# Optimization experiments

Measured on AMD Instinct MI355X. Metric: run time of the kernel, lower is better.

The kernel has to match this reference:

```python
import jax, jax.numpy as jnp
import numpy as np

TEMPERATURE = 1.0  # module default current_temperature
TOP_K = 2
NUM_EXPERTS = 64
EPS = 1e-10


def setup_inputs() -> dict:
    key = jax.random.key(0)
    k1, k2 = jax.random.split(key)
    x = jax.random.normal(k1, (4, 4096, 2048), dtype=jnp.float32)
    # nn.Linear(d_model, num_experts) weight has shape [num_experts, d_model]
    W_gate = jax.random.normal(k2, (NUM_EXPERTS, 2048), dtype=jnp.float32) * (1.0 / np.sqrt(2048))
    return {"x": x, "W_gate": W_gate}


def reference(x, W_gate):
    # Gate GEMM: [B,S,D] x [E,D] -> [B,S,E]
    logits = jnp.einsum("bsd,ed->bse", x, W_gate)
    scaled = logits / TEMPERATURE
    # Full distribution over experts (for load-balancing loss)
    router_probs = jax.nn.softmax(scaled, axis=-1)
    # Top-k selection over the expert dim, then renormalize via softmax
    top_k_logits, top_k_indices = jax.lax.top_k(scaled, TOP_K)  # [B,S,K]
    top_k_weights = jax.nn.softmax(top_k_logits, axis=-1)
    # Routing stats (no-grad in torch; plain values here)
    entropy = -jnp.sum(router_probs * jnp.log(router_probs + EPS), axis=-1)
    routing_entropy = entropy.mean()
    selection_confidence = top_k_weights[:, :, 0].mean()
    counts = jnp.zeros((NUM_EXPERTS,), dtype=x.dtype).at[top_k_indices.reshape(-1)].add(1.0)
    expert_utilization = counts / (counts.sum() + EPS)
    return (top_k_weights, top_k_indices, router_probs,
            routing_entropy, selection_confidence, expert_utilization)
```

## Files before the change

### kernel.cpp

```cpp
#include <hip/hip_runtime.h>
#include <math.h>

#define NTOK 16384
#define DIM 2048
#define NEXP 64
#define KG 4
#define NC 16
#define WTOK 32
#define BTOK 128

#define OFF_W    0
#define OFF_I    32768
#define OFF_P    65536
#define OFF_ENT  1114112
#define OFF_CONF 1114113
#define OFF_UTIL 1114114

#define PLG_OFF  196608
#define PLG_STRIDE 1048576
#define WS_NEED_STRIDED (786432ull + 16777216ull)

typedef short s16x8 __attribute__((ext_vector_type(8)));
typedef float f32x4 __attribute__((ext_vector_type(4)));

__device__ __forceinline__ unsigned short f2bf(float v) {
    unsigned u = __builtin_bit_cast(unsigned, v);
    u = u + 0x7FFFu + ((u >> 16) & 1u);
    return (unsigned short)(u >> 16);
}
__device__ __forceinline__ float bf2f(unsigned short b) {
    return __builtin_bit_cast(float, (unsigned)b << 16);
}

__device__ __forceinline__ void gload16(const void* g, void* l) {
    __builtin_amdgcn_global_load_lds(
        (const __attribute__((address_space(1))) unsigned int*)g,
        (__attribute__((address_space(3))) unsigned int*)l, 16, 0, 0);
}

__global__ void router_wsplit(const float* __restrict__ Wg, uint4* __restrict__ wsp,
                              float* __restrict__ out) {
    const int bid = blockIdx.x;
    const int tid = threadIdx.x;
    const int c   = bid >> 2;
    const int gt  = (bid & 3) * 64 + tid;
    if (c == 0 && gt < 66) out[OFF_ENT + gt] = 0.0f;
    const int nt = gt >> 6, l = gt & 63;
    const int e  = 16 * nt + (l & 15);
    const int k0 = 32 * c + 8 * (l >> 4);
    const float* src = Wg + (size_t)e * DIM + k0;
    float4 a = *(const float4*)src;
    float4 b = *(const float4*)(src + 4);
    float v[8] = {a.x, a.y, a.z, a.w, b.x, b.y, b.z, b.w};
    unsigned short H[8], M[8], L[8];
    #pragma unroll
    for (int j = 0; j < 8; ++j) {
        H[j] = f2bf(v[j]);  float r = v[j] - bf2f(H[j]);
        M[j] = f2bf(r);     r = r - bf2f(M[j]);
        L[j] = f2bf(r);
    }
    uint4 ph, pm, pl;
    ph.x = H[0] | ((unsigned)H[1] << 16); ph.y = H[2] | ((unsigned)H[3] << 16);
    ph.z = H[4] | ((unsigned)H[5] << 16); ph.w = H[6] | ((unsigned)H[7] << 16);
    pm.x = M[0] | ((unsigned)M[1] << 16); pm.y = M[2] | ((unsigned)M[3] << 16);
    pm.z = M[4] | ((unsigned)M[5] << 16); pm.w = M[6] | ((unsigned)M[7] << 16);
    pl.x = L[0] | ((unsigned)L[1] << 16); pl.y = L[2] | ((unsigned)L[3] << 16);
    pl.z = L[4] | ((unsigned)L[5] << 16); pl.w = L[6] | ((unsigned)L[7] << 16);
    const int idx = c * 256 + gt;
    wsp[idx]         = ph;
    wsp[16384 + idx] = pm;
    wsp[32768 + idx] = pl;
}

__global__ void router_zero(float* __restrict__ p) {
    ((float4*)p)[blockIdx.x * 256 + threadIdx.x] = make_float4(0.f, 0.f, 0.f, 0.f);
}

#define CONVA3(a0_, a1_) {                                               \
    float xv[8];                                                         \
    xv[0]=a0_.x; xv[1]=a0_.y; xv[2]=a0_.z; xv[3]=a0_.w;                  \
    xv[4]=a1_.x; xv[5]=a1_.y; xv[6]=a1_.z; xv[7]=a1_.w;                  \
    _Pragma("unroll")                                                    \
    for (int j = 0; j < 8; ++j) {                                        \
        unsigned u_  = __builtin_bit_cast(unsigned, xv[j]);              \
        unsigned hb_ = u_ & 0xFFFF0000u;                                 \
        float    r_  = xv[j] - __builtin_bit_cast(float, hb_);           \
        unsigned mb_ = __builtin_bit_cast(unsigned, r_) & 0xFFFF0000u;   \
        float    r2_ = r_ - __builtin_bit_cast(float, mb_);              \
        unsigned lb_ = __builtin_bit_cast(unsigned, r2_);                \
        ah[j] = (short)(hb_ >> 16);                                      \
        am[j] = (short)(mb_ >> 16);                                      \
        al[j] = (short)(lb_ >> 16);                                      \
    } }

#define MF(A_, B_, C_) __builtin_amdgcn_mfma_f32_16x16x32_bf16(A_, B_, C_, 0, 0, 0)
#define BC(q_) __builtin_bit_cast(s16x8, q_)

#define STAGE(c_) { _Pragma("unroll")                                    \
    for (int i_ = 0; i_ < 4; ++i_) {                                     \
        const int tau_ = 8 * i_ + (l >> 3);                              \
        const int gs_  = ((l & 7) >> 1) ^ (tau_ & 3);                    \
        gload16(xw + (size_t)tau_ * DIM + (c_) * 32 + gs_ * 8 + (l & 1) * 4, \
                &ring[wv][(c_) & 3][8 * i_][0]);                         \
    } }

#define READA(tt_, c_) {                                                 \
    const int tau_ = (tt_) * 16 + tr;                                    \
    const int sl_  = qd ^ (tau_ & 3);                                    \
    const uint4* row_ = &ring[wv][(c_) & 3][tau_][0];                    \
    float4 a0_ = __builtin_bit_cast(float4, row_[2 * sl_]);              \
    float4 a1_ = __builtin_bit_cast(float4, row_[2 * sl_ + 1]);          \
    CONVA3(a0_, a1_);                                                    \
    }

#define LOADW12(W_, c_) { const int b_ = (kg * NC + (c_)) * 256 + l;     \
    W_[0] = wq[b_];          W_[1] = wq[b_ + 64];                        \
    W_[2] = wq[b_ + 128];    W_[3] = wq[b_ + 192];                       \
    W_[4] = wq[16384 + b_];       W_[5] = wq[16384 + b_ + 64];           \
    W_[6] = wq[16384 + b_ + 128]; W_[7] = wq[16384 + b_ + 192];          \
    W_[8] = wq[32768 + b_];       W_[9] = wq[32768 + b_ + 64];           \
    W_[10] = wq[32768 + b_ + 128]; W_[11] = wq[32768 + b_ + 192]; }

#define PR4(F_, W_, o_, Q0_, Q1_, Q2_, Q3_) {                            \
    Q0_ = MF(F_, BC(W_[(o_) + 0]), Q0_);                                 \
    Q1_ = MF(F_, BC(W_[(o_) + 1]), Q1_);                                 \
    Q2_ = MF(F_, BC(W_[(o_) + 2]), Q2_);                                 \
    Q3_ = MF(F_, BC(W_[(o_) + 3]), Q3_); }

#define COMPUTE24(W_, Q0_, Q1_, Q2_, Q3_) {                              \
    PR4(ah, W_, 0, Q0_, Q1_, Q2_, Q3_);                                  \
    PR4(am, W_, 0, Q0_, Q1_, Q2_, Q3_);                                  \
    PR4(ah, W_, 4, Q0_, Q1_, Q2_, Q3_);                                  \
    PR4(am, W_, 4, Q0_, Q1_, Q2_, Q3_);                                  \
    PR4(ah, W_, 8, Q0_, Q1_, Q2_, Q3_);                                  \
    PR4(al, W_, 0, Q0_, Q1_, Q2_, Q3_); }

#define PHASE(c_, W_) {                                                  \
    if ((c_) + 3 < NC) STAGE((c_) + 3);                                  \
    asm volatile("s_waitcnt vmcnt(8)" ::: "memory");                     \
    __builtin_amdgcn_sched_barrier(0);                                   \
    READA(0, c_);                                                        \
    COMPUTE24(W_, q00, q01, q02, q03);                                   \
    READA(1, c_);                                                        \
    COMPUTE24(W_, q10, q11, q12, q13);                                   \
    if ((c_) + 2 < NC) LOADW12(W_, (c_) + 2);                            \
    }

template<bool STRIDED>
__global__ __launch_bounds__(256, 2) void router_main(
    const float* __restrict__ x, const uint4* __restrict__ wq,
    float* __restrict__ plg)
{
    __shared__ __align__(16) uint4 ring[4][4][WTOK][8];

    const int tid = threadIdx.x;
    const int l   = tid & 63;
    const int wv  = tid >> 6;
    const int tr  = l & 15;
    const int qd  = l >> 4;
    const int kg  = blockIdx.x & 3;
    const int bt0 = (blockIdx.x >> 2) * BTOK;
    const int t0w = bt0 + wv * WTOK;

    const float* xw = x + (size_t)t0w * DIM + kg * (NC * 32);

    f32x4 q00 = (f32x4)(0.f), q01 = (f32x4)(0.f), q02 = (f32x4)(0.f), q03 = (f32x4)(0.f);
    f32x4 q10 = (f32x4)(0.f), q11 = (f32x4)(0.f), q12 = (f32x4)(0.f), q13 = (f32x4)(0.f);
    s16x8 ah, am, al;
    uint4 wA[12], wB[12];

    STAGE(0); STAGE(1); STAGE(2);
    LOADW12(wA, 0); LOADW12(wB, 1);

    #pragma unroll
    for (int c = 0; c < NC; c += 2) {
        PHASE(c, wA);
        PHASE(c + 1, wB);
    }

    float* dst = STRIDED ? (plg + (size_t)kg * PLG_STRIDE) : plg;
#define STACC(acc_, tt_, nt_) { _Pragma("unroll")                        \
    for (int r = 0; r < 4; ++r) {                                        \
        int tok = t0w + (tt_) * 16 + 4 * qd + r;                         \
        int ex_ = (nt_) * 16 + tr;                                       \
        if constexpr (STRIDED) dst[(size_t)tok * 64 + ex_] = acc_[r];    \
        else atomicAdd(&dst[(size_t)tok * 64 + ex_], acc_[r]);           \
    } }
    STACC(q00, 0, 0); STACC(q01, 0, 1); STACC(q02, 0, 2); STACC(q03, 0, 3);
    STACC(q10, 1, 0); STACC(q11, 1, 1); STACC(q12, 1, 2); STACC(q13, 1, 3);
#undef STACC
}

__device__ __forceinline__ void merge2(float& m1, int& i1, float& m2, int& i2,
                                       float om1, int oi1, float om2, int oi2) {
    bool of = (om1 > m1) || (om1 == m1 && oi1 < i1);
    float n1, n2; int j1, j2;
    if (of) {
        n1 = om1; j1 = oi1;
        bool s = (m1 > om2) || (m1 == om2 && i1 < oi2);
        n2 = s ? m1 : om2; j2 = s ? i1 : oi2;
    } else {
        n1 = m1; j1 = i1;
        bool s = (om1 > m2) || (om1 == m2 && oi1 < i2);
        n2 = s ? om1 : m2; j2 = s ? oi1 : i2;
    }
    m1 = n1; i1 = j1; m2 = n2; i2 = j2;
}

template<int NPART>
__global__ void router_post(const float* __restrict__ plg, float* __restrict__ out) {
    __shared__ float s_ent, s_conf, s_cnt[NEXP];
    const int tid  = threadIdx.x;
    const int lane = tid & 63;
    const int wv   = tid >> 6;
    if (tid == 0) { s_ent = 0.f; s_conf = 0.f; }
    if (tid < NEXP) s_cnt[tid] = 0.f;
    __syncthreads();

    const int tb = blockIdx.x * 32 + wv * 8;
    float entA = 0.f, confA = 0.f;

    for (int k = 0; k < 8; ++k) {
        const int t = tb + k;
        float lgv = 0.f;
        #pragma unroll
        for (int p = 0; p < NPART; ++p)
            lgv += plg[(size_t)p * PLG_STRIDE + (size_t)t * 64 + lane];

        float m1 = lgv, m2 = -INFINITY;
        int   i1 = lane, i2 = 127;
        #pragma unroll
        for (int off = 32; off >= 1; off >>= 1) {
            float om1 = __shfl_xor(m1, off);
            int   oi1 = __shfl_xor(i1, off);
            float om2 = __shfl_xor(m2, off);
            int   oi2 = __shfl_xor(i2, off);
            merge2(m1, i1, m2, i2, om1, oi1, om2, oi2);
        }
        float d  = lgv - m1;
        float ex = __expf(d);
        float ss = ex, ts = d * ex;
        #pragma unroll
        for (int off = 32; off >= 1; off >>= 1) {
            ss += __shfl_xor(ss, off);
            ts += __shfl_xor(ts, off);
        }
        float rs = 1.0f / ss;
        out[OFF_P + (size_t)t * 64 + lane] = ex * rs;
        if (lane == 0) {
            float H  = logf(ss) - ts * rs;
            float e2 = __expf(m2 - m1);
            float rn = 1.0f / (1.0f + e2);
            *(float2*)&out[OFF_W + 2 * t] = make_float2(rn, e2 * rn);
            *(float2*)&out[OFF_I + 2 * t] = make_float2((float)i1, (float)i2);
            entA  += H;
            confA += rn;
            atomicAdd(&s_cnt[i1], 1.0f);
            atomicAdd(&s_cnt[i2], 1.0f);
        }
    }
    if (lane == 0) { atomicAdd(&s_ent, entA); atomicAdd(&s_conf, confA); }
    __syncthreads();
    if (tid == 0) {
        atomicAdd(&out[OFF_ENT],  s_ent  * (1.0f / 16384.0f));
        atomicAdd(&out[OFF_CONF], s_conf * (1.0f / 16384.0f));
    }
    if (tid < NEXP)
        atomicAdd(&out[OFF_UTIL + tid], s_cnt[tid] * (1.0f / 32768.0f));
}

extern "C" void kernel_launch(void* const* d_in, const int* in_sizes, int n_in,
                              void* d_out, int out_size, void* d_ws, size_t ws_size,
                              hipStream_t stream) {
    const float* x  = (const float*)d_in[0];
    const float* Wg = (const float*)d_in[1];
    float* out = (float*)d_out;
    float* plg = (float*)d_ws + PLG_OFF;
    (void)in_sizes; (void)n_in; (void)out_size;

    router_wsplit<<<dim3(256), dim3(64), 0, stream>>>(Wg, (uint4*)d_ws, out);
    if (ws_size >= WS_NEED_STRIDED) {
        router_main<true><<<dim3((NTOK / BTOK) * KG), dim3(256), 0, stream>>>(
            x, (const uint4*)d_ws, plg);
        router_post<KG><<<dim3(512), dim3(256), 0, stream>>>(plg, out);
    } else {
        router_zero<<<dim3(1024), dim3(256), 0, stream>>>(plg);
        router_main<false><<<dim3((NTOK / BTOK) * KG), dim3(256), 0, stream>>>(
            x, (const uint4*)d_ws, plg);
        router_post<1><<<dim3(512), dim3(256), 0, stream>>>(plg, out);
    }
}
```

Baseline: 240.5 us.

## Fuse gate GEMM and softmax/top-k epilogue into one kernel with in-block split-K

Replaces the three-kernel pipeline (weight pre-split, split-K GEMM writing partial logits to workspace, post-processing kernel) with a single kernel. Each block handles 32 tokens, its four waves split the K dimension, reduce their partial logits through shared memory, then run softmax, top-2, entropy and utilisation directly. W is now loaded as fp32 and split into three bf16 parts inside the loop instead of once up front. This drops the partial-logit round trip through global memory and two launches, at the cost of redundant W conversion per block, a shallower double-buffered x ring, and serialized shared-memory reductions.

```diff
diff --git a/kernel.cpp b/kernel.cpp
--- a/kernel.cpp
+++ b/kernel.cpp
@@ -4,10 +4,8 @@
 #define NTOK 16384
 #define DIM 2048
 #define NEXP 64
-#define KG 4
-#define NC 16
 #define WTOK 32
-#define BTOK 128
+#define NCW 16
 
 #define OFF_W    0
 #define OFF_I    32768
@@ -16,10 +14,6 @@
 #define OFF_CONF 1114113
 #define OFF_UTIL 1114114
 
-#define PLG_OFF  196608
-#define PLG_STRIDE 1048576
-#define WS_NEED_STRIDED (786432ull + 16777216ull)
-
 typedef short s16x8 __attribute__((ext_vector_type(8)));
 typedef float f32x4 __attribute__((ext_vector_type(4)));
 
@@ -38,45 +32,19 @@
         (__attribute__((address_space(3))) unsigned int*)l, 16, 0, 0);
 }
 
-__global__ void router_wsplit(const float* __restrict__ Wg, uint4* __restrict__ wsp,
-                              float* __restrict__ out) {
-    const int bid = blockIdx.x;
-    const int tid = threadIdx.x;
-    const int c   = bid >> 2;
-    const int gt  = (bid & 3) * 64 + tid;
-    if (c == 0 && gt < 66) out[OFF_ENT + gt] = 0.0f;
-    const int nt = gt >> 6, l = gt & 63;
-    const int e  = 16 * nt + (l & 15);
-    const int k0 = 32 * c + 8 * (l >> 4);
-    const float* src = Wg + (size_t)e * DIM + k0;
-    float4 a = *(const float4*)src;
-    float4 b = *(const float4*)(src + 4);
-    float v[8] = {a.x, a.y, a.z, a.w, b.x, b.y, b.z, b.w};
-    unsigned short H[8], M[8], L[8];
-    #pragma unroll
-    for (int j = 0; j < 8; ++j) {
-        H[j] = f2bf(v[j]);  float r = v[j] - bf2f(H[j]);
-        M[j] = f2bf(r);     r = r - bf2f(M[j]);
-        L[j] = f2bf(r);
-    }
-    uint4 ph, pm, pl;
-    ph.x = H[0] | ((unsigned)H[1] << 16); ph.y = H[2] | ((unsigned)H[3] << 16);
-    ph.z = H[4] | ((unsigned)H[5] << 16); ph.w = H[6] | ((unsigned)H[7] << 16);
-    pm.x = M[0] | ((unsigned)M[1] << 16); pm.y = M[2] | ((unsigned)M[3] << 16);
-    pm.z = M[4] | ((unsigned)M[5] << 16); pm.w = M[6] | ((unsigned)M[7] << 16);
-    pl.x = L[0] | ((unsigned)L[1] << 16); pl.y = L[2] | ((unsigned)L[3] << 16);
-    pl.z = L[4] | ((unsigned)L[5] << 16); pl.w = L[6] | ((unsigned)L[7] << 16);
-    const int idx = c * 256 + gt;
-    wsp[idx]         = ph;
-    wsp[16384 + idx] = pm;
-    wsp[32768 + idx] = pl;
-}
-
-__global__ void router_zero(float* __restrict__ p) {
-    ((float4*)p)[blockIdx.x * 256 + threadIdx.x] = make_float4(0.f, 0.f, 0.f, 0.f);
-}
-
-#define CONVA3(a0_, a1_) {                                               \
+__global__ void router_init(float* __restrict__ out) {
+    if (threadIdx.x < 66) out[OFF_ENT + threadIdx.x] = 0.0f;
+}
+
+#define STAGE(c_) do { _Pragma("unroll")                                 \
+    for (int i_ = 0; i_ < 4; ++i_) {                                     \
+        const int tau_ = 8 * i_ + (l >> 3);                              \
+        const int gs_  = ((l & 7) >> 1) ^ (tau_ & 3);                    \
+        gload16(xw + (size_t)tau_ * DIM + (c_) * 32 + gs_ * 8 + (l & 1) * 4, \
+                &ring[wv][(c_) & 1][8 * i_][0]);                         \
+    } } while (0)
+
+#define CONVA3(a0_, a1_) do {                                            \
     float xv[8];                                                         \
     xv[0]=a0_.x; xv[1]=a0_.y; xv[2]=a0_.z; xv[3]=a0_.w;                  \
     xv[4]=a1_.x; xv[5]=a1_.y; xv[6]=a1_.z; xv[7]=a1_.w;                  \
@@ -91,105 +59,53 @@
         ah[j] = (short)(hb_ >> 16);                                      \
         am[j] = (short)(mb_ >> 16);                                      \
         al[j] = (short)(lb_ >> 16);                                      \
-    } }
-
-#define MF(A_, B_, C_) __builtin_amdgcn_mfma_f32_16x16x32_bf16(A_, B_, C_, 0, 0, 0)
-#define BC(q_) __builtin_bit_cast(s16x8, q_)
-
-#define STAGE(c_) { _Pragma("unroll")                                    \
-    for (int i_ = 0; i_ < 4; ++i_) {                                     \
-        const int tau_ = 8 * i_ + (l >> 3);                              \
-        const int gs_  = ((l & 7) >> 1) ^ (tau_ & 3);                    \
-        gload16(xw + (size_t)tau_ * DIM + (c_) * 32 + gs_ * 8 + (l & 1) * 4, \
-                &ring[wv][(c_) & 3][8 * i_][0]);                         \
-    } }
-
-#define READA(tt_, c_) {                                                 \
+    } } while (0)
+
+#define READA(tt_, c_) do {                                              \
     const int tau_ = (tt_) * 16 + tr;                                    \
     const int sl_  = qd ^ (tau_ & 3);                                    \
-    const uint4* row_ = &ring[wv][(c_) & 3][tau_][0];                    \
+    const uint4* row_ = &ring[wv][(c_) & 1][tau_][0];                    \
     float4 a0_ = __builtin_bit_cast(float4, row_[2 * sl_]);              \
     float4 a1_ = __builtin_bit_cast(float4, row_[2 * sl_ + 1]);          \
     CONVA3(a0_, a1_);                                                    \
-    }
-
-#define LOADW12(W_, c_) { const int b_ = (kg * NC + (c_)) * 256 + l;     \
-    W_[0] = wq[b_];          W_[1] = wq[b_ + 64];                        \
-    W_[2] = wq[b_ + 128];    W_[3] = wq[b_ + 192];                       \
-    W_[4] = wq[16384 + b_];       W_[5] = wq[16384 + b_ + 64];           \
-    W_[6] = wq[16384 + b_ + 128]; W_[7] = wq[16384 + b_ + 192];          \
-    W_[8] = wq[32768 + b_];       W_[9] = wq[32768 + b_ + 64];           \
-    W_[10] = wq[32768 + b_ + 128]; W_[11] = wq[32768 + b_ + 192]; }
-
-#define PR4(F_, W_, o_, Q0_, Q1_, Q2_, Q3_) {                            \
-    Q0_ = MF(F_, BC(W_[(o_) + 0]), Q0_);                                 \
-    Q1_ = MF(F_, BC(W_[(o_) + 1]), Q1_);                                 \
-    Q2_ = MF(F_, BC(W_[(o_) + 2]), Q2_);                                 \
-    Q3_ = MF(F_, BC(W_[(o_) + 3]), Q3_); }
-
-#define COMPUTE24(W_, Q0_, Q1_, Q2_, Q3_) {                              \
-    PR4(ah, W_, 0, Q0_, Q1_, Q2_, Q3_);                                  \
-    PR4(am, W_, 0, Q0_, Q1_, Q2_, Q3_);                                  \
-    PR4(ah, W_, 4, Q0_, Q1_, Q2_, Q3_);                                  \
-    PR4(am, W_, 4, Q0_, Q1_, Q2_, Q3_);                                  \
-    PR4(ah, W_, 8, Q0_, Q1_, Q2_, Q3_);                                  \
-    PR4(al, W_, 0, Q0_, Q1_, Q2_, Q3_); }
-
-#define PHASE(c_, W_) {                                                  \
-    if ((c_) + 3 < NC) STAGE((c_) + 3);                                  \
-    asm volatile("s_waitcnt vmcnt(8)" ::: "memory");                     \
-    __builtin_amdgcn_sched_barrier(0);                                   \
-    READA(0, c_);                                                        \
-    COMPUTE24(W_, q00, q01, q02, q03);                                   \
-    READA(1, c_);                                                        \
-    COMPUTE24(W_, q10, q11, q12, q13);                                   \
-    if ((c_) + 2 < NC) LOADW12(W_, (c_) + 2);                            \
-    }
-
-template<bool STRIDED>
-__global__ __launch_bounds__(256, 2) void router_main(
-    const float* __restrict__ x, const uint4* __restrict__ wq,
-    float* __restrict__ plg)
-{
-    __shared__ __align__(16) uint4 ring[4][4][WTOK][8];
-
-    const int tid = threadIdx.x;
-    const int l   = tid & 63;
-    const int wv  = tid >> 6;
-    const int tr  = l & 15;
-    const int qd  = l >> 4;
-    const int kg  = blockIdx.x & 3;
-    const int bt0 = (blockIdx.x >> 2) * BTOK;
-    const int t0w = bt0 + wv * WTOK;
-
-    const float* xw = x + (size_t)t0w * DIM + kg * (NC * 32);
-
-    f32x4 q00 = (f32x4)(0.f), q01 = (f32x4)(0.f), q02 = (f32x4)(0.f), q03 = (f32x4)(0.f);
-    f32x4 q10 = (f32x4)(0.f), q11 = (f32x4)(0.f), q12 = (f32x4)(0.f), q13 = (f32x4)(0.f);
-    s16x8 ah, am, al;
-    uint4 wA[12], wB[12];
-
-    STAGE(0); STAGE(1); STAGE(2);
-    LOADW12(wA, 0); LOADW12(wB, 1);
-
-    #pragma unroll
-    for (int c = 0; c < NC; c += 2) {
-        PHASE(c, wA);
-        PHASE(c + 1, wB);
-    }
-
-    float* dst = STRIDED ? (plg + (size_t)kg * PLG_STRIDE) : plg;
-#define STACC(acc_, tt_, nt_) { _Pragma("unroll")                        \
-    for (int r = 0; r < 4; ++r) {                                        \
-        int tok = t0w + (tt_) * 16 + 4 * qd + r;                         \
-        int ex_ = (nt_) * 16 + tr;                                       \
-        if constexpr (STRIDED) dst[(size_t)tok * 64 + ex_] = acc_[r];    \
-        else atomicAdd(&dst[(size_t)tok * 64 + ex_], acc_[r]);           \
-    } }
-    STACC(q00, 0, 0); STACC(q01, 0, 1); STACC(q02, 0, 2); STACC(q03, 0, 3);
-    STACC(q10, 1, 0); STACC(q11, 1, 1); STACC(q12, 1, 2); STACC(q13, 1, 3);
-#undef STACC
-}
+    } while (0)
+
+#define LOADWF(W_, c_) do { _Pragma("unroll")                            \
+    for (int nt_ = 0; nt_ < 4; ++nt_) {                                  \
+        const float* p_ = wsrc + (size_t)nt_ * 16 * DIM + (c_) * 32;     \
+        W_[2 * nt_]     = *(const float4*)(p_);                          \
+        W_[2 * nt_ + 1] = *(const float4*)(p_ + 4);                      \
+    } } while (0)
+
+#define CONVW(a_, b_, BH_, BM_, BL_) do {                                \
+    float wv8[8];                                                        \
+    wv8[0]=a_.x; wv8[1]=a_.y; wv8[2]=a_.z; wv8[3]=a_.w;                  \
+    wv8[4]=b_.x; wv8[5]=b_.y; wv8[6]=b_.z; wv8[7]=b_.w;                  \
+    _Pragma("unroll")                                                    \
+    for (int j = 0; j < 8; ++j) {                                        \
+        unsigned short h_ = f2bf(wv8[j]);                                \
+        float r_  = wv8[j] - bf2f(h_);                                   \
+        unsigned short m_ = f2bf(r_);                                    \
+        float r2_ = r_ - bf2f(m_);                                       \
+        unsigned short lo_ = f2bf(r2_);                                  \
+        BH_[j] = (short)h_; BM_[j] = (short)m_; BL_[j] = (short)lo_;     \
+    } } while (0)
+
+#define MF(A_, B_, C_) __builtin_amdgcn_mfma_f32_16x16x32_bf16(A_, B_, C_, 0, 0, 0)
+
+#define PR4(F_, B_, Q0_, Q1_, Q2_, Q3_) do {                             \
+    Q0_ = MF(F_, B_[0], Q0_);                                            \
+    Q1_ = MF(F_, B_[1], Q1_);                                            \
+    Q2_ = MF(F_, B_[2], Q2_);                                            \
+    Q3_ = MF(F_, B_[3], Q3_); } while (0)
+
+#define COMPUTE24(Q0_, Q1_, Q2_, Q3_) do {                               \
+    PR4(ah, bh, Q0_, Q1_, Q2_, Q3_);                                     \
+    PR4(am, bh, Q0_, Q1_, Q2_, Q3_);                                     \
+    PR4(ah, bm, Q0_, Q1_, Q2_, Q3_);                                     \
+    PR4(am, bm, Q0_, Q1_, Q2_, Q3_);                                     \
+    PR4(ah, bl, Q0_, Q1_, Q2_, Q3_);                                     \
+    PR4(al, bh, Q0_, Q1_, Q2_, Q3_); } while (0)
 
 __device__ __forceinline__ void merge2(float& m1, int& i1, float& m2, int& i2,
                                        float om1, int oi1, float om2, int oi2) {
@@ -207,28 +123,87 @@
     m1 = n1; i1 = j1; m2 = n2; i2 = j2;
 }
 
-template<int NPART>
-__global__ void router_post(const float* __restrict__ plg, float* __restrict__ out) {
+__global__ __launch_bounds__(256, 2) void router_main(
+    const float* __restrict__ x, const float* __restrict__ Wg,
+    float* __restrict__ out)
+{
+    __shared__ __align__(16) uint4 ring[4][2][WTOK][8];
+    __shared__ float lg[WTOK][NEXP + 1];
     __shared__ float s_ent, s_conf, s_cnt[NEXP];
-    const int tid  = threadIdx.x;
-    const int lane = tid & 63;
-    const int wv   = tid >> 6;
+
+    const int tid = threadIdx.x;
+    const int l   = tid & 63;
+    const int wv  = tid >> 6;
+    const int tr  = l & 15;
+    const int qd  = l >> 4;
+    const int t0  = blockIdx.x * WTOK;
+
     if (tid == 0) { s_ent = 0.f; s_conf = 0.f; }
     if (tid < NEXP) s_cnt[tid] = 0.f;
-    __syncthreads();
-
-    const int tb = blockIdx.x * 32 + wv * 8;
+
+    const float* xw   = x  + (size_t)t0 * DIM + wv * (NCW * 32);
+    const float* wsrc = Wg + (size_t)tr * DIM + wv * (NCW * 32) + 8 * qd;
+
+    f32x4 q00 = (f32x4)(0.f), q01 = (f32x4)(0.f), q02 = (f32x4)(0.f), q03 = (f32x4)(0.f);
+    f32x4 q10 = (f32x4)(0.f), q11 = (f32x4)(0.f), q12 = (f32x4)(0.f), q13 = (f32x4)(0.f);
+    s16x8 ah, am, al;
+    s16x8 bh[4], bm[4], bl[4];
+    float4 wA[8], wB[8];
+
+    STAGE(0);
+    LOADWF(wA, 0); LOADWF(wB, 1);
+
+    #pragma unroll
+    for (int c = 0; c < NCW; ++c) {
+        if (c + 1 < NCW) STAGE(c + 1);
+        if (c == NCW - 1) { asm volatile("s_waitcnt vmcnt(0)" ::: "memory"); }
+        else              { asm volatile("s_waitcnt vmcnt(12)" ::: "memory"); }
+        __builtin_amdgcn_sched_barrier(0);
+        {
+            float4* wc = (c & 1) ? wB : wA;
+            #pragma unroll
+            for (int nt = 0; nt < 4; ++nt)
+                CONVW(wc[2 * nt], wc[2 * nt + 1], bh[nt], bm[nt], bl[nt]);
+        }
+        READA(0, c);
+        COMPUTE24(q00, q01, q02, q03);
+        READA(1, c);
+        COMPUTE24(q10, q11, q12, q13);
+        {
+            float4* wn = (c & 1) ? wB : wA;
+            if (c + 2 < NCW) LOADWF(wn, c + 2);
+        }
+    }
+
+#define WRROWS(op_) { _Pragma("unroll")                                  \
+    for (int r = 0; r < 4; ++r) {                                        \
+        lg[4 * qd + r][0 * 16 + tr]      op_ q00[r];                     \
+        lg[4 * qd + r][1 * 16 + tr]      op_ q01[r];                     \
+        lg[4 * qd + r][2 * 16 + tr]      op_ q02[r];                     \
+        lg[4 * qd + r][3 * 16 + tr]      op_ q03[r];                     \
+        lg[16 + 4 * qd + r][0 * 16 + tr] op_ q10[r];                     \
+        lg[16 + 4 * qd + r][1 * 16 + tr] op_ q11[r];                     \
+        lg[16 + 4 * qd + r][2 * 16 + tr] op_ q12[r];                     \
+        lg[16 + 4 * qd + r][3 * 16 + tr] op_ q13[r];                     \
+    } }
+    if (wv == 0) WRROWS(=);
+    __syncthreads();
+    if (wv == 1) WRROWS(+=);
+    __syncthreads();
+    if (wv == 2) WRROWS(+=);
+    __syncthreads();
+    if (wv == 3) WRROWS(+=);
+    __syncthreads();
+#undef WRROWS
+
     float entA = 0.f, confA = 0.f;
-
+    #pragma unroll
     for (int k = 0; k < 8; ++k) {
-        const int t = tb + k;
-        float lgv = 0.f;
-        #pragma unroll
-        for (int p = 0; p < NPART; ++p)
-            lgv += plg[(size_t)p * PLG_STRIDE + (size_t)t * 64 + lane];
+        const int t = wv * 8 + k;
+        float lgv = lg[t][l];
 
         float m1 = lgv, m2 = -INFINITY;
-        int   i1 = lane, i2 = 127;
+        int   i1 = l, i2 = 127;
         #pragma unroll
         for (int off = 32; off >= 1; off >>= 1) {
             float om1 = __shfl_xor(m1, off);
@@ -246,21 +221,22 @@
             ts += __shfl_xor(ts, off);
         }
         float rs = 1.0f / ss;
-        out[OFF_P + (size_t)t * 64 + lane] = ex * rs;
-        if (lane == 0) {
+        out[OFF_P + (size_t)(t0 + t) * NEXP + l] = ex * rs;
+        if (l == 0) {
             float H  = logf(ss) - ts * rs;
             float e2 = __expf(m2 - m1);
             float rn = 1.0f / (1.0f + e2);
-            *(float2*)&out[OFF_W + 2 * t] = make_float2(rn, e2 * rn);
-            *(float2*)&out[OFF_I + 2 * t] = make_float2((float)i1, (float)i2);
+            *(float2*)&out[OFF_W + 2 * (t0 + t)] = make_float2(rn, e2 * rn);
+            *(float2*)&out[OFF_I + 2 * (t0 + t)] = make_float2((float)i1, (float)i2);
             entA  += H;
             confA += rn;
             atomicAdd(&s_cnt[i1], 1.0f);
             atomicAdd(&s_cnt[i2], 1.0f);
         }
     }
-    if (lane == 0) { atomicAdd(&s_ent, entA); atomicAdd(&s_conf, confA); }
-    __syncthreads();
+    if (l == 0) { atomicAdd(&s_ent, entA); atomicAdd(&s_conf, confA); }
+    __syncthreads();
+
     if (tid == 0) {
         atomicAdd(&out[OFF_ENT],  s_ent  * (1.0f / 16384.0f));
         atomicAdd(&out[OFF_CONF], s_conf * (1.0f / 16384.0f));
@@ -275,18 +251,8 @@
     const float* x  = (const float*)d_in[0];
     const float* Wg = (const float*)d_in[1];
     float* out = (float*)d_out;
-    float* plg = (float*)d_ws + PLG_OFF;
-    (void)in_sizes; (void)n_in; (void)out_size;
-
-    router_wsplit<<<dim3(256), dim3(64), 0, stream>>>(Wg, (uint4*)d_ws, out);
-    if (ws_size >= WS_NEED_STRIDED) {
-        router_main<true><<<dim3((NTOK / BTOK) * KG), dim3(256), 0, stream>>>(
-            x, (const uint4*)d_ws, plg);
-        router_post<KG><<<dim3(512), dim3(256), 0, stream>>>(plg, out);
-    } else {
-        router_zero<<<dim3(1024), dim3(256), 0, stream>>>(plg);
-        router_main<false><<<dim3((NTOK / BTOK) * KG), dim3(256), 0, stream>>>(
-            x, (const uint4*)d_ws, plg);
-        router_post<1><<<dim3(512), dim3(256), 0, stream>>>(plg, out);
-    }
-}
+    (void)in_sizes; (void)n_in; (void)out_size; (void)d_ws; (void)ws_size;
+
+    router_init<<<dim3(1), dim3(128), 0, stream>>>(out);
+    router_main<<<dim3(NTOK / WTOK), dim3(256), 0, stream>>>(x, Wg, out);
+}
```

Result: no change. 236.8 us (-1.5%).
